# Kernel optimization log

Hardware: AMD Instinct MI355X
Metric: run time of the kernel (lower is better)

## Reference

```python
import jax, jax.numpy as jnp
import numpy as np

B, N, T, S = 32, 102400, 64, 1600
PI = float(np.pi)
EPS = 1e-12  # numerical guard inside sqrt for cdist (diagonal is exactly 0)


def _cdist(a, b):
    # a: (..., P, 3), b: (..., Q, 3) -> (..., P, Q) euclidean distances
    sq = jnp.sum((a[..., :, None, :] - b[..., None, :, :]) ** 2, axis=-1)
    return jnp.sqrt(sq + EPS)


def _rigid_t(alpha, trans, sz, center):
    # alpha, trans: (B, T, 3). Returns XYZ (B,T,3,3), translation (B,T,3).
    c, s = jnp.cos(alpha), jnp.sin(alpha)
    z = jnp.zeros_like(c[..., 0]); o = jnp.ones_like(c[..., 0])
    X = jnp.stack([c[..., 0], -s[..., 0], z, s[..., 0], c[..., 0], z, z, z, o], -1).reshape(*alpha.shape[:2], 3, 3)
    Y = jnp.stack([c[..., 1], z, s[..., 1], z, o, z, -s[..., 1], z, c[..., 1]], -1).reshape(*alpha.shape[:2], 3, 3)
    Z = jnp.stack([o, z, z, z, c[..., 2], -s[..., 2], z, s[..., 2], c[..., 2]], -1).reshape(*alpha.shape[:2], 3, 3)
    XYZ = jnp.einsum('btij,btjk,btkl->btil', X, Y, Z)
    eye = jnp.eye(3, dtype=alpha.dtype)
    Tt = trans * sz[None, None, :] + jnp.einsum('m,btmk->btk', center, eye[None, None] - XYZ)
    return XYZ, Tt


def setup_inputs():
    key = jax.random.key(0)
    ks = jax.random.split(key, 6)
    x = jax.random.normal(ks[0], (B, 6, N), jnp.float32)
    w1 = jax.random.normal(ks[1], (3 * N, 32), jnp.float32) * 0.005
    b1 = jnp.zeros((32,), jnp.float32)
    w2 = jax.random.normal(ks[2], (32, 6 * T), jnp.float32) * 0.05
    b2 = jnp.zeros((6 * T,), jnp.float32)
    A = jax.random.normal(ks[3], (6, N), jnp.float32)
    mask = jax.random.uniform(ks[4], (T, T), jnp.float32)
    sz = jnp.array([128.0, 128.0, 64.0], jnp.float32)
    tess = jnp.arange(N, dtype=jnp.int32).reshape(T, S)  # equal-size partition
    return {'x': x, 'w1': w1, 'b1': b1, 'w2': w2, 'b2': b2, 'A': A, 'mask': mask, 'sz': sz, 'tess': tess}


def reference(x, w1, b1, w2, b2, A, mask, sz, tess):
    center = sz / 2.0
    # localization MLP on flattened xyz coords: (B, 3N) -> (B, T, 6)
    xflat = x[:, :3, :].reshape(B, 3 * N)
    h = jax.nn.relu(xflat @ w1 + b1)
    z_l = jnp.tanh(h @ w2 + b2).reshape(B, T, 6)
    # NOTE: original code uses z_l[:, :, 3:] for BOTH angles and translation
    r_, t_ = _rigid_t(PI * z_l[:, :, 3:], z_l[:, :, 3:], sz, center)
    x3 = x[:, :3, :]
    xg = x3[:, :, tess]  # gather: (B, 3, T, S)
    # out[b,j,p,n] = sum_k r_[b,p,k,j] * xg[b,k,p,n]  (matches einsum 'bkt,bkn->btn')
    rot = jnp.einsum('bpkj,bkpn->bjpn', r_, xg) + t_.transpose(0, 2, 1)[:, :, :, None]
    # scatter back into full point cloud (tess partitions N)
    X3 = jnp.zeros_like(x3).at[:, :, tess.reshape(-1)].set(rot.reshape(B, 3, N))
    X_t = jnp.concatenate([X3, x[:, 3:, :]], axis=1)  # colors pass through identity
    # regularizer on per-piece centroids
    pts_1 = A[:3][:, tess].mean(axis=2).T                 # (T, 3)
    pts_2 = X3[:, :, tess].mean(axis=3).transpose(0, 2, 1)  # (B, T, 3)
    diff = _cdist(pts_1, pts_1)[None] - _cdist(pts_2, pts_2)
    reg = jnp.sum((mask[None] * diff) ** 2, axis=(1, 2))  # (B,)
    return X_t, reg
```

## Files before the change

### kernel.cpp

```cpp
#include <hip/hip_runtime.h>
#include <hip/hip_bf16.h>
#include <math.h>

#define BB 32
#define NN 102400
#define TT 64
#define SS 1600
#define K3N (3 * NN)
#define KC 128
#define G1 512
#define NCHUNK (K3N / KC)
#define XPAD 132
#define PI_F 3.14159265358979323846f

__global__ __launch_bounds__(256) void k1_gemm(const float* __restrict__ x,
                                               const float* __restrict__ w1,
                                               float* __restrict__ h_part) {
    __shared__ float xs[32 * XPAD];
    __shared__ float ws1[KC * 32];
    const int tid = threadIdx.x;
    const int b = tid >> 3, cq = tid & 7;
    float a0 = 0.f, a1 = 0.f, a2 = 0.f, a3 = 0.f;

    for (int chunk = blockIdx.x; chunk < NCHUNK; chunk += G1) {
        const int k0 = chunk * KC;
        for (int i = tid; i < 32 * 32; i += 256) {
            const int bb = i >> 5, k4 = i & 31;
            const float4 v = *(const float4*)(x + (size_t)bb * 6 * NN + k0 + k4 * 4);
            *(float4*)(xs + bb * XPAD + k4 * 4) = v;
        }
        for (int i = tid; i < (KC * 32) / 4; i += 256) {
            *(float4*)(ws1 + i * 4) = *(const float4*)(w1 + (size_t)k0 * 32 + i * 4);
        }
        __syncthreads();
        const float* xrow = xs + b * XPAD;
        #pragma unroll 8
        for (int k4 = 0; k4 < KC / 4; ++k4) {
            const float4 xv = *(const float4*)(xrow + k4 * 4);
            #pragma unroll
            for (int j = 0; j < 4; ++j) {
                const float xj = j == 0 ? xv.x : (j == 1 ? xv.y : (j == 2 ? xv.z : xv.w));
                const float4 wv = *(const float4*)(ws1 + (k4 * 4 + j) * 32 + cq * 4);
                a0 = fmaf(xj, wv.x, a0);
                a1 = fmaf(xj, wv.y, a1);
                a2 = fmaf(xj, wv.z, a2);
                a3 = fmaf(xj, wv.w, a3);
            }
        }
        __syncthreads();
    }
    float4 r; r.x = a0; r.y = a1; r.z = a2; r.w = a3;
    *(float4*)(h_part + (size_t)blockIdx.x * 1024 + tid * 4) = r;
}

__global__ __launch_bounds__(256) void kb_fused(const float* __restrict__ h_part,
                                                const float* __restrict__ b1,
                                                const float* __restrict__ w2,
                                                const float* __restrict__ b2,
                                                const float* __restrict__ sz,
                                                const float* __restrict__ A,
                                                const int* __restrict__ tess,
                                                float* __restrict__ RT,
                                                float* __restrict__ pts1) {
    const int blk = blockIdx.x;
    if (blk < BB) {
        const int bb = blk;
        __shared__ float part[8][32];
        __shared__ float hsh[32];
        const int c = threadIdx.x & 31, g = threadIdx.x >> 5;
        float s = 0.f;
        for (int j = g; j < G1; j += 8) s += h_part[(size_t)j * 1024 + bb * 32 + c];
        part[g][c] = s;
        __syncthreads();
        if (threadIdx.x < 32) {
            float acc = 0.f;
            #pragma unroll
            for (int g2 = 0; g2 < 8; ++g2) acc += part[g2][threadIdx.x];
            hsh[threadIdx.x] = fmaxf(acc + b1[threadIdx.x], 0.f);
        }
        __syncthreads();
        const int t = threadIdx.x;
        if (t < TT) {
            float z[3];
            #pragma unroll
            for (int j = 0; j < 3; ++j) {
                const int col = 6 * t + 3 + j;
                float s2 = b2[col];
                #pragma unroll 8
                for (int cc = 0; cc < 32; ++cc) s2 = fmaf(hsh[cc], w2[cc * 384 + col], s2);
                z[j] = tanhf(s2);
            }
            float c0, s0, c1, s1, c2, s2v;
            sincosf(PI_F * z[0], &s0, &c0);
            sincosf(PI_F * z[1], &s1, &c1);
            sincosf(PI_F * z[2], &s2v, &c2);
            const float R00 = c0 * c1;
            const float R01 = -s0 * c2 + c0 * s1 * s2v;
            const float R02 = s0 * s2v + c0 * s1 * c2;
            const float R10 = s0 * c1;
            const float R11 = c0 * c2 + s0 * s1 * s2v;
            const float R12 = -c0 * s2v + s0 * s1 * c2;
            const float R20 = -s1;
            const float R21 = c1 * s2v;
            const float R22 = c1 * c2;
            const float szx = sz[0], szy = sz[1], szz = sz[2];
            const float cx = 0.5f * szx, cy = 0.5f * szy, cz = 0.5f * szz;
            const float T0 = z[0] * szx + cx - (cx * R00 + cy * R10 + cz * R20);
            const float T1 = z[1] * szy + cy - (cx * R01 + cy * R11 + cz * R21);
            const float T2 = z[2] * szz + cz - (cx * R02 + cy * R12 + cz * R22);
            float* o = RT + (bb * TT + t) * 12;
            o[0] = R00; o[1] = R10; o[2]  = R20; o[3]  = T0;
            o[4] = R01; o[5] = R11; o[6]  = R21; o[7]  = T1;
            o[8] = R02; o[9] = R12; o[10] = R22; o[11] = T2;
        }
    } else {
        const int t = blk - BB;
        const int* tr = tess + t * SS;
        float s0 = 0.f, s1 = 0.f, s2 = 0.f;
        for (int s = threadIdx.x; s < SS; s += 256) {
            const int idx = tr[s];
            s0 += A[idx]; s1 += A[NN + idx]; s2 += A[2 * NN + idx];
        }
        #pragma unroll
        for (int o = 32; o > 0; o >>= 1) {
            s0 += __shfl_down(s0, o, 64);
            s1 += __shfl_down(s1, o, 64);
            s2 += __shfl_down(s2, o, 64);
        }
        __shared__ float red[4 * 3];
        const int lane = threadIdx.x & 63, wv = threadIdx.x >> 6;
        if (lane == 0) { red[wv * 3] = s0; red[wv * 3 + 1] = s1; red[wv * 3 + 2] = s2; }
        __syncthreads();
        if (threadIdx.x < 3) {
            const float s = red[threadIdx.x] + red[3 + threadIdx.x] + red[6 + threadIdx.x] + red[9 + threadIdx.x];
            pts1[t * 3 + threadIdx.x] = s * (1.0f / SS);
        }
    }
}

__global__ __launch_bounds__(256) void k3_transform(const float* __restrict__ x,
                                                    const int* __restrict__ tess,
                                                    const float* __restrict__ RT,
                                                    float* __restrict__ out,
                                                    float* __restrict__ pts2) {
    const int blk = blockIdx.x;
    const int b = blk / TT, t = blk % TT;
    const float* p = RT + blk * 12;
    const float M00 = p[0], M01 = p[1], M02 = p[2], T0 = p[3];
    const float M10 = p[4], M11 = p[5], M12 = p[6], T1 = p[7];
    const float M20 = p[8], M21 = p[9], M22 = p[10], T2 = p[11];
    const float* xb = x + (size_t)b * 6 * NN;
    float* ob = out + (size_t)b * 6 * NN;
    const int* tr = tess + t * SS;
    float s0 = 0.f, s1 = 0.f, s2 = 0.f;
    for (int s = threadIdx.x; s < SS; s += 256) {
        const int idx = tr[s];
        const float x0 = xb[idx], x1 = xb[NN + idx], x2 = xb[2 * NN + idx];
        const float y0 = fmaf(M00, x0, fmaf(M01, x1, fmaf(M02, x2, T0)));
        const float y1 = fmaf(M10, x0, fmaf(M11, x1, fmaf(M12, x2, T1)));
        const float y2 = fmaf(M20, x0, fmaf(M21, x1, fmaf(M22, x2, T2)));
        ob[idx] = y0; ob[NN + idx] = y1; ob[2 * NN + idx] = y2;
        s0 += y0; s1 += y1; s2 += y2;
    }
    const int n0 = t * SS;
    for (int i = threadIdx.x; i < 1200; i += 256) {
        const int ch = i / 400, r = i - ch * 400;
        const size_t off = (size_t)(3 + ch) * NN + n0 + r * 4;
        *(float4*)(ob + off) = *(const float4*)(xb + off);
    }
    #pragma unroll
    for (int o = 32; o > 0; o >>= 1) {
        s0 += __shfl_down(s0, o, 64);
        s1 += __shfl_down(s1, o, 64);
        s2 += __shfl_down(s2, o, 64);
    }
    __shared__ float red[4 * 3];
    const int lane = threadIdx.x & 63, wv = threadIdx.x >> 6;
    if (lane == 0) { red[wv * 3] = s0; red[wv * 3 + 1] = s1; red[wv * 3 + 2] = s2; }
    __syncthreads();
    if (threadIdx.x < 3) {
        const float s = red[threadIdx.x] + red[3 + threadIdx.x] + red[6 + threadIdx.x] + red[9 + threadIdx.x];
        pts2[blk * 3 + threadIdx.x] = s * (1.0f / SS);
    }
}

__global__ __launch_bounds__(256) void k5_reg(const float* __restrict__ pts1,
                                              const float* __restrict__ pts2,
                                              const float* __restrict__ mask,
                                              float* __restrict__ out) {
    const int b = blockIdx.x;
    __shared__ float p1[TT * 3], p2[TT * 3];
    for (int i = threadIdx.x; i < TT * 3; i += 256) {
        p1[i] = pts1[i];
        p2[i] = pts2[b * TT * 3 + i];
    }
    __syncthreads();
    float acc = 0.f;
    for (int pr = threadIdx.x; pr < TT * TT; pr += 256) {
        const int t = pr >> 6, u = pr & 63;
        float dx = p1[t * 3] - p1[u * 3];
        float dy = p1[t * 3 + 1] - p1[u * 3 + 1];
        float dz = p1[t * 3 + 2] - p1[u * 3 + 2];
        const float d1 = sqrtf(dx * dx + dy * dy + dz * dz + 1e-12f);
        dx = p2[t * 3] - p2[u * 3];
        dy = p2[t * 3 + 1] - p2[u * 3 + 1];
        dz = p2[t * 3 + 2] - p2[u * 3 + 2];
        const float d2 = sqrtf(dx * dx + dy * dy + dz * dz + 1e-12f);
        const float d = mask[pr] * (d1 - d2);
        acc = fmaf(d, d, acc);
    }
    #pragma unroll
    for (int o = 32; o > 0; o >>= 1) acc += __shfl_down(acc, o, 64);
    __shared__ float red[4];
    const int lane = threadIdx.x & 63, wv = threadIdx.x >> 6;
    if (lane == 0) red[wv] = acc;
    __syncthreads();
    if (threadIdx.x == 0) {
        out[(size_t)BB * 6 * NN + b] = red[0] + red[1] + red[2] + red[3];
    }
}

extern "C" void kernel_launch(void* const* d_in, const int* in_sizes, int n_in,
                              void* d_out, int out_size, void* d_ws, size_t ws_size,
                              hipStream_t stream) {
    const float* x    = (const float*)d_in[0];
    const float* w1   = (const float*)d_in[1];
    const float* b1   = (const float*)d_in[2];
    const float* w2   = (const float*)d_in[3];
    const float* b2   = (const float*)d_in[4];
    const float* A    = (const float*)d_in[5];
    const float* mask = (const float*)d_in[6];
    const float* sz   = (const float*)d_in[7];
    const int*   tess = (const int*)d_in[8];
    float* out = (float*)d_out;
    float* ws  = (float*)d_ws;

    float* h_part = ws;
    float* RT     = h_part + G1 * 1024;
    float* pts2   = RT + BB * TT * 12;
    float* pts1   = pts2 + BB * TT * 3;

    k1_gemm<<<G1, 256, 0, stream>>>(x, w1, h_part);
    kb_fused<<<BB + TT, 256, 0, stream>>>(h_part, b1, w2, b2, sz, A, tess, RT, pts1);
    k3_transform<<<BB * TT, 256, 0, stream>>>(x, tess, RT, out, pts2);
    k5_reg<<<BB, 256, 0, stream>>>(pts1, pts2, mask, out);
}
```

Measured before the change: 90.07 us.

## Retile first GEMM with 4x8 register tiles, split-K across lanes, larger grid

```diff
diff --git a/kernel.cpp b/kernel.cpp
--- a/kernel.cpp
+++ b/kernel.cpp
@@ -7,50 +7,84 @@
 #define TT 64
 #define SS 1600
 #define K3N (3 * NN)
-#define KC 128
-#define G1 512
+#define KC 64
 #define NCHUNK (K3N / KC)
-#define XPAD 132
+#define XP 68
+#define WP 40
 #define PI_F 3.14159265358979323846f
 
 __global__ __launch_bounds__(256) void k1_gemm(const float* __restrict__ x,
                                                const float* __restrict__ w1,
                                                float* __restrict__ h_part) {
-    __shared__ float xs[32 * XPAD];
-    __shared__ float ws1[KC * 32];
+    __shared__ float xs[32 * XP];
+    __shared__ float ws1[KC * WP];
     const int tid = threadIdx.x;
-    const int b = tid >> 3, cq = tid & 7;
-    float a0 = 0.f, a1 = 0.f, a2 = 0.f, a3 = 0.f;
-
-    for (int chunk = blockIdx.x; chunk < NCHUNK; chunk += G1) {
+    const int ks = tid & 7;
+    const int tile = tid >> 3;
+    const int bg = tile & 7;
+    const int cg = tile >> 3;
+    float acc[4][8];
+    #pragma unroll
+    for (int j = 0; j < 4; ++j)
+        #pragma unroll
+        for (int c = 0; c < 8; ++c) acc[j][c] = 0.f;
+
+    const int nblk = gridDim.x;
+    for (int chunk = blockIdx.x; chunk < NCHUNK; chunk += nblk) {
         const int k0 = chunk * KC;
-        for (int i = tid; i < 32 * 32; i += 256) {
-            const int bb = i >> 5, k4 = i & 31;
-            const float4 v = *(const float4*)(x + (size_t)bb * 6 * NN + k0 + k4 * 4);
-            *(float4*)(xs + bb * XPAD + k4 * 4) = v;
-        }
-        for (int i = tid; i < (KC * 32) / 4; i += 256) {
-            *(float4*)(ws1 + i * 4) = *(const float4*)(w1 + (size_t)k0 * 32 + i * 4);
-        }
-        __syncthreads();
-        const float* xrow = xs + b * XPAD;
-        #pragma unroll 8
-        for (int k4 = 0; k4 < KC / 4; ++k4) {
-            const float4 xv = *(const float4*)(xrow + k4 * 4);
+        {
+            const int bb = tid >> 4, k4 = (tid & 15) * 4;
+            const float4 v0 = *(const float4*)(x + (size_t)bb * 6 * NN + k0 + k4);
+            *(float4*)(xs + bb * XP + k4) = v0;
+            const float4 v1 = *(const float4*)(x + (size_t)(bb + 16) * 6 * NN + k0 + k4);
+            *(float4*)(xs + (bb + 16) * XP + k4) = v1;
+        }
+        {
+            const int r = tid >> 3, c4 = (tid & 7) * 4;
+            *(float4*)(ws1 + r * WP + c4) = *(const float4*)(w1 + (size_t)(k0 + r) * 32 + c4);
+            *(float4*)(ws1 + (r + 32) * WP + c4) = *(const float4*)(w1 + (size_t)(k0 + r + 32) * 32 + c4);
+        }
+        __syncthreads();
+        #pragma unroll
+        for (int i = 0; i < 8; ++i) {
+            const int k = ks + 8 * i;
+            const float4 wa = *(const float4*)(ws1 + k * WP + cg * 8);
+            const float4 wb = *(const float4*)(ws1 + k * WP + cg * 8 + 4);
+            float xv[4];
+            #pragma unroll
+            for (int j = 0; j < 4; ++j) xv[j] = xs[(bg + 8 * j) * XP + k];
             #pragma unroll
             for (int j = 0; j < 4; ++j) {
-                const float xj = j == 0 ? xv.x : (j == 1 ? xv.y : (j == 2 ? xv.z : xv.w));
-                const float4 wv = *(const float4*)(ws1 + (k4 * 4 + j) * 32 + cq * 4);
-                a0 = fmaf(xj, wv.x, a0);
-                a1 = fmaf(xj, wv.y, a1);
-                a2 = fmaf(xj, wv.z, a2);
-                a3 = fmaf(xj, wv.w, a3);
+                acc[j][0] = fmaf(xv[j], wa.x, acc[j][0]);
+                acc[j][1] = fmaf(xv[j], wa.y, acc[j][1]);
+                acc[j][2] = fmaf(xv[j], wa.z, acc[j][2]);
+                acc[j][3] = fmaf(xv[j], wa.w, acc[j][3]);
+                acc[j][4] = fmaf(xv[j], wb.x, acc[j][4]);
+                acc[j][5] = fmaf(xv[j], wb.y, acc[j][5]);
+                acc[j][6] = fmaf(xv[j], wb.z, acc[j][6]);
+                acc[j][7] = fmaf(xv[j], wb.w, acc[j][7]);
             }
         }
         __syncthreads();
     }
-    float4 r; r.x = a0; r.y = a1; r.z = a2; r.w = a3;
-    *(float4*)(h_part + (size_t)blockIdx.x * 1024 + tid * 4) = r;
+    #pragma unroll
+    for (int off = 1; off < 8; off <<= 1) {
+        #pragma unroll
+        for (int j = 0; j < 4; ++j)
+            #pragma unroll
+            for (int c = 0; c < 8; ++c)
+                acc[j][c] += __shfl_xor(acc[j][c], off, 64);
+    }
+    if (ks == 0) {
+        float* hp = h_part + (size_t)blockIdx.x * 1024;
+        #pragma unroll
+        for (int j = 0; j < 4; ++j) {
+            const int b = bg + 8 * j;
+            #pragma unroll
+            for (int c = 0; c < 8; ++c)
+                hp[b * 32 + cg * 8 + c] = acc[j][c];
+        }
+    }
 }
 
 __global__ __launch_bounds__(256) void kb_fused(const float* __restrict__ h_part,
@@ -61,7 +95,8 @@
                                                 const float* __restrict__ A,
                                                 const int* __restrict__ tess,
                                                 float* __restrict__ RT,
-                                                float* __restrict__ pts1) {
+                                                float* __restrict__ pts1,
+                                                int g1) {
     const int blk = blockIdx.x;
     if (blk < BB) {
         const int bb = blk;
@@ -69,7 +104,7 @@
         __shared__ float hsh[32];
         const int c = threadIdx.x & 31, g = threadIdx.x >> 5;
         float s = 0.f;
-        for (int j = g; j < G1; j += 8) s += h_part[(size_t)j * 1024 + bb * 32 + c];
+        for (int j = g; j < g1; j += 8) s += h_part[(size_t)j * 1024 + bb * 32 + c];
         part[g][c] = s;
         __syncthreads();
         if (threadIdx.x < 32) {
@@ -235,13 +270,16 @@
     float* out = (float*)d_out;
     float* ws  = (float*)d_ws;
 
+    int g1 = 1024;
+    while ((size_t)(g1 * 1024 + 2048 * 12 + 2048 * 3 + 192) * 4 > ws_size && g1 > 128) g1 >>= 1;
+
     float* h_part = ws;
-    float* RT     = h_part + G1 * 1024;
+    float* RT     = h_part + (size_t)g1 * 1024;
     float* pts2   = RT + BB * TT * 12;
     float* pts1   = pts2 + BB * TT * 3;
 
-    k1_gemm<<<G1, 256, 0, stream>>>(x, w1, h_part);
-    kb_fused<<<BB + TT, 256, 0, stream>>>(h_part, b1, w2, b2, sz, A, tess, RT, pts1);
+    k1_gemm<<<g1, 256, 0, stream>>>(x, w1, h_part);
+    kb_fused<<<BB + TT, 256, 0, stream>>>(h_part, b1, w2, b2, sz, A, tess, RT, pts1, g1);
     k3_transform<<<BB * TT, 256, 0, stream>>>(x, tess, RT, out, pts2);
     k5_reg<<<BB, 256, 0, stream>>>(pts1, pts2, mask, out);
 }
```

Result: slower. 95.83 us (+6.4%).

## Restructure GEMM as per-wave split-K and fuse color copy and centroids into it

Applied to the files above, without the earlier changes.

```diff
diff --git a/kernel.cpp b/kernel.cpp
--- a/kernel.cpp
+++ b/kernel.cpp
@@ -7,134 +7,149 @@
 #define TT 64
 #define SS 1600
 #define K3N (3 * NN)
-#define KC 128
-#define G1 512
-#define NCHUNK (K3N / KC)
-#define XPAD 132
+#define CPB 512
 #define PI_F 3.14159265358979323846f
 
-__global__ __launch_bounds__(256) void k1_gemm(const float* __restrict__ x,
+__global__ __launch_bounds__(256) void k1_mega(const float* __restrict__ x,
                                                const float* __restrict__ w1,
-                                               float* __restrict__ h_part) {
-    __shared__ float xs[32 * XPAD];
-    __shared__ float ws1[KC * 32];
+                                               const float* __restrict__ A,
+                                               const int* __restrict__ tess,
+                                               float* __restrict__ h_part,
+                                               float* __restrict__ out,
+                                               float* __restrict__ pts1,
+                                               int nw) {
     const int tid = threadIdx.x;
-    const int b = tid >> 3, cq = tid & 7;
-    float a0 = 0.f, a1 = 0.f, a2 = 0.f, a3 = 0.f;
-
-    for (int chunk = blockIdx.x; chunk < NCHUNK; chunk += G1) {
-        const int k0 = chunk * KC;
-        for (int i = tid; i < 32 * 32; i += 256) {
-            const int bb = i >> 5, k4 = i & 31;
-            const float4 v = *(const float4*)(x + (size_t)bb * 6 * NN + k0 + k4 * 4);
-            *(float4*)(xs + bb * XPAD + k4 * 4) = v;
-        }
-        for (int i = tid; i < (KC * 32) / 4; i += 256) {
-            *(float4*)(ws1 + i * 4) = *(const float4*)(w1 + (size_t)k0 * 32 + i * 4);
-        }
+    const int gemmBlocks = nw >> 2;
+    if (blockIdx.x < gemmBlocks) {
+        const int wid = blockIdx.x * 4 + (tid >> 6);
+        const int lane = tid & 63;
+        const int b = lane & 31, kh = lane >> 5;
+        const int kstart = (int)(((long)wid * K3N) / nw);
+        const int kend   = (int)(((long)(wid + 1) * K3N) / nw);
+
+        float acc[32];
+        #pragma unroll
+        for (int c = 0; c < 32; ++c) acc[c] = 0.f;
+
+        const float* xp = x + (size_t)b * 6 * NN + kstart + kh;
+        const float* wp = w1 + (size_t)(kstart + kh) * 32;
+
+        #pragma unroll 2
+        for (int k0 = kstart; k0 < kend; k0 += 2) {
+            const float xv = *xp;
+            float4 w[8];
+            #pragma unroll
+            for (int q = 0; q < 8; ++q) w[q] = *(const float4*)(wp + 4 * q);
+            #pragma unroll
+            for (int q = 0; q < 8; ++q) {
+                acc[4 * q + 0] = fmaf(xv, w[q].x, acc[4 * q + 0]);
+                acc[4 * q + 1] = fmaf(xv, w[q].y, acc[4 * q + 1]);
+                acc[4 * q + 2] = fmaf(xv, w[q].z, acc[4 * q + 2]);
+                acc[4 * q + 3] = fmaf(xv, w[q].w, acc[4 * q + 3]);
+            }
+            xp += 2;
+            wp += 64;
+        }
+        #pragma unroll
+        for (int c = 0; c < 32; ++c) acc[c] += __shfl_xor(acc[c], 32, 64);
+        if (kh == 0) {
+            float* hp = h_part + (size_t)wid * 1024 + b * 32;
+            #pragma unroll
+            for (int q = 0; q < 8; ++q) {
+                float4 v;
+                v.x = acc[4 * q + 0]; v.y = acc[4 * q + 1];
+                v.z = acc[4 * q + 2]; v.w = acc[4 * q + 3];
+                *(float4*)(hp + 4 * q) = v;
+            }
+        }
+    } else if (blockIdx.x < gemmBlocks + CPB) {
+        const int cb = blockIdx.x - gemmBlocks;
+        for (int i = cb * 256 + tid; i < 2457600; i += CPB * 256) {
+            const int b = i / 76800;
+            const int rem = i - b * 76800;
+            const size_t off = (size_t)b * (6 * NN) + K3N + (size_t)rem * 4;
+            *(float4*)(out + off) = *(const float4*)(x + off);
+        }
+    } else {
+        const int t = blockIdx.x - gemmBlocks - CPB;
+        const int* tr = tess + t * SS;
+        float s0 = 0.f, s1 = 0.f, s2 = 0.f;
+        for (int s = tid; s < SS; s += 256) {
+            const int idx = tr[s];
+            s0 += A[idx]; s1 += A[NN + idx]; s2 += A[2 * NN + idx];
+        }
+        #pragma unroll
+        for (int o = 32; o > 0; o >>= 1) {
+            s0 += __shfl_down(s0, o, 64);
+            s1 += __shfl_down(s1, o, 64);
+            s2 += __shfl_down(s2, o, 64);
+        }
+        __shared__ float red[4 * 3];
+        const int lane = tid & 63, wv = tid >> 6;
+        if (lane == 0) { red[wv * 3] = s0; red[wv * 3 + 1] = s1; red[wv * 3 + 2] = s2; }
         __syncthreads();
-        const float* xrow = xs + b * XPAD;
-        #pragma unroll 8
-        for (int k4 = 0; k4 < KC / 4; ++k4) {
-            const float4 xv = *(const float4*)(xrow + k4 * 4);
-            #pragma unroll
-            for (int j = 0; j < 4; ++j) {
-                const float xj = j == 0 ? xv.x : (j == 1 ? xv.y : (j == 2 ? xv.z : xv.w));
-                const float4 wv = *(const float4*)(ws1 + (k4 * 4 + j) * 32 + cq * 4);
-                a0 = fmaf(xj, wv.x, a0);
-                a1 = fmaf(xj, wv.y, a1);
-                a2 = fmaf(xj, wv.z, a2);
-                a3 = fmaf(xj, wv.w, a3);
-            }
-        }
-        __syncthreads();
-    }
-    float4 r; r.x = a0; r.y = a1; r.z = a2; r.w = a3;
-    *(float4*)(h_part + (size_t)blockIdx.x * 1024 + tid * 4) = r;
-}
-
-__global__ __launch_bounds__(256) void kb_fused(const float* __restrict__ h_part,
+        if (tid < 3) {
+            const float s = red[tid] + red[3 + tid] + red[6 + tid] + red[9 + tid];
+            pts1[t * 3 + tid] = s * (1.0f / SS);
+        }
+    }
+}
+
+__global__ __launch_bounds__(256) void kb_rigid(const float* __restrict__ h_part,
                                                 const float* __restrict__ b1,
                                                 const float* __restrict__ w2,
                                                 const float* __restrict__ b2,
                                                 const float* __restrict__ sz,
-                                                const float* __restrict__ A,
-                                                const int* __restrict__ tess,
                                                 float* __restrict__ RT,
-                                                float* __restrict__ pts1) {
-    const int blk = blockIdx.x;
-    if (blk < BB) {
-        const int bb = blk;
-        __shared__ float part[8][32];
-        __shared__ float hsh[32];
-        const int c = threadIdx.x & 31, g = threadIdx.x >> 5;
-        float s = 0.f;
-        for (int j = g; j < G1; j += 8) s += h_part[(size_t)j * 1024 + bb * 32 + c];
-        part[g][c] = s;
-        __syncthreads();
-        if (threadIdx.x < 32) {
-            float acc = 0.f;
-            #pragma unroll
-            for (int g2 = 0; g2 < 8; ++g2) acc += part[g2][threadIdx.x];
-            hsh[threadIdx.x] = fmaxf(acc + b1[threadIdx.x], 0.f);
-        }
-        __syncthreads();
-        const int t = threadIdx.x;
-        if (t < TT) {
-            float z[3];
-            #pragma unroll
-            for (int j = 0; j < 3; ++j) {
-                const int col = 6 * t + 3 + j;
-                float s2 = b2[col];
-                #pragma unroll 8
-                for (int cc = 0; cc < 32; ++cc) s2 = fmaf(hsh[cc], w2[cc * 384 + col], s2);
-                z[j] = tanhf(s2);
-            }
-            float c0, s0, c1, s1, c2, s2v;
-            sincosf(PI_F * z[0], &s0, &c0);
-            sincosf(PI_F * z[1], &s1, &c1);
-            sincosf(PI_F * z[2], &s2v, &c2);
-            const float R00 = c0 * c1;
-            const float R01 = -s0 * c2 + c0 * s1 * s2v;
-            const float R02 = s0 * s2v + c0 * s1 * c2;
-            const float R10 = s0 * c1;
-            const float R11 = c0 * c2 + s0 * s1 * s2v;
-            const float R12 = -c0 * s2v + s0 * s1 * c2;
-            const float R20 = -s1;
-            const float R21 = c1 * s2v;
-            const float R22 = c1 * c2;
-            const float szx = sz[0], szy = sz[1], szz = sz[2];
-            const float cx = 0.5f * szx, cy = 0.5f * szy, cz = 0.5f * szz;
-            const float T0 = z[0] * szx + cx - (cx * R00 + cy * R10 + cz * R20);
-            const float T1 = z[1] * szy + cy - (cx * R01 + cy * R11 + cz * R21);
-            const float T2 = z[2] * szz + cz - (cx * R02 + cy * R12 + cz * R22);
-            float* o = RT + (bb * TT + t) * 12;
-            o[0] = R00; o[1] = R10; o[2]  = R20; o[3]  = T0;
-            o[4] = R01; o[5] = R11; o[6]  = R21; o[7]  = T1;
-            o[8] = R02; o[9] = R12; o[10] = R22; o[11] = T2;
-        }
-    } else {
-        const int t = blk - BB;
-        const int* tr = tess + t * SS;
-        float s0 = 0.f, s1 = 0.f, s2 = 0.f;
-        for (int s = threadIdx.x; s < SS; s += 256) {
-            const int idx = tr[s];
-            s0 += A[idx]; s1 += A[NN + idx]; s2 += A[2 * NN + idx];
-        }
-        #pragma unroll
-        for (int o = 32; o > 0; o >>= 1) {
-            s0 += __shfl_down(s0, o, 64);
-            s1 += __shfl_down(s1, o, 64);
-            s2 += __shfl_down(s2, o, 64);
-        }
-        __shared__ float red[4 * 3];
-        const int lane = threadIdx.x & 63, wv = threadIdx.x >> 6;
-        if (lane == 0) { red[wv * 3] = s0; red[wv * 3 + 1] = s1; red[wv * 3 + 2] = s2; }
-        __syncthreads();
-        if (threadIdx.x < 3) {
-            const float s = red[threadIdx.x] + red[3 + threadIdx.x] + red[6 + threadIdx.x] + red[9 + threadIdx.x];
-            pts1[t * 3 + threadIdx.x] = s * (1.0f / SS);
-        }
+                                                int nw) {
+    const int bb = blockIdx.x;
+    __shared__ float part[8][32];
+    __shared__ float hsh[32];
+    const int c = threadIdx.x & 31, g = threadIdx.x >> 5;
+    float s = 0.f;
+    for (int j = g; j < nw; j += 8) s += h_part[(size_t)j * 1024 + bb * 32 + c];
+    part[g][c] = s;
+    __syncthreads();
+    if (threadIdx.x < 32) {
+        float acc = 0.f;
+        #pragma unroll
+        for (int g2 = 0; g2 < 8; ++g2) acc += part[g2][threadIdx.x];
+        hsh[threadIdx.x] = fmaxf(acc + b1[threadIdx.x], 0.f);
+    }
+    __syncthreads();
+    const int t = threadIdx.x;
+    if (t < TT) {
+        float z[3];
+        #pragma unroll
+        for (int j = 0; j < 3; ++j) {
+            const int col = 6 * t + 3 + j;
+            float s2 = b2[col];
+            #pragma unroll 8
+            for (int cc = 0; cc < 32; ++cc) s2 = fmaf(hsh[cc], w2[cc * 384 + col], s2);
+            z[j] = tanhf(s2);
+        }
+        float c0, s0, c1, s1, c2, s2v;
+        sincosf(PI_F * z[0], &s0, &c0);
+        sincosf(PI_F * z[1], &s1, &c1);
+        sincosf(PI_F * z[2], &s2v, &c2);
+        const float R00 = c0 * c1;
+        const float R01 = -s0 * c2 + c0 * s1 * s2v;
+        const float R02 = s0 * s2v + c0 * s1 * c2;
+        const float R10 = s0 * c1;
+        const float R11 = c0 * c2 + s0 * s1 * s2v;
+        const float R12 = -c0 * s2v + s0 * s1 * c2;
+        const float R20 = -s1;
+        const float R21 = c1 * s2v;
+        const float R22 = c1 * c2;
+        const float szx = sz[0], szy = sz[1], szz = sz[2];
+        const float cx = 0.5f * szx, cy = 0.5f * szy, cz = 0.5f * szz;
+        const float T0 = z[0] * szx + cx - (cx * R00 + cy * R10 + cz * R20);
+        const float T1 = z[1] * szy + cy - (cx * R01 + cy * R11 + cz * R21);
+        const float T2 = z[2] * szz + cz - (cx * R02 + cy * R12 + cz * R22);
+        float* o = RT + (bb * TT + t) * 12;
+        o[0] = R00; o[1] = R10; o[2]  = R20; o[3]  = T0;
+        o[4] = R01; o[5] = R11; o[6]  = R21; o[7]  = T1;
+        o[8] = R02; o[9] = R12; o[10] = R22; o[11] = T2;
     }
 }
 
@@ -162,12 +177,6 @@
         ob[idx] = y0; ob[NN + idx] = y1; ob[2 * NN + idx] = y2;
         s0 += y0; s1 += y1; s2 += y2;
     }
-    const int n0 = t * SS;
-    for (int i = threadIdx.x; i < 1200; i += 256) {
-        const int ch = i / 400, r = i - ch * 400;
-        const size_t off = (size_t)(3 + ch) * NN + n0 + r * 4;
-        *(float4*)(ob + off) = *(const float4*)(xb + off);
-    }
     #pragma unroll
     for (int o = 32; o > 0; o >>= 1) {
         s0 += __shfl_down(s0, o, 64);
@@ -235,13 +244,16 @@
     float* out = (float*)d_out;
     float* ws  = (float*)d_ws;
 
+    int nw = 2048;
+    while ((size_t)((size_t)nw * 1024 + 2048 * 12 + 2048 * 3 + 192) * 4 > ws_size && nw > 512) nw >>= 1;
+
     float* h_part = ws;
-    float* RT     = h_part + G1 * 1024;
+    float* RT     = h_part + (size_t)nw * 1024;
     float* pts2   = RT + BB * TT * 12;
     float* pts1   = pts2 + BB * TT * 3;
 
-    k1_gemm<<<G1, 256, 0, stream>>>(x, w1, h_part);
-    kb_fused<<<BB + TT, 256, 0, stream>>>(h_part, b1, w2, b2, sz, A, tess, RT, pts1);
+    k1_mega<<<(nw >> 2) + CPB + TT, 256, 0, stream>>>(x, w1, A, tess, h_part, out, pts1, nw);
+    kb_rigid<<<BB, 256, 0, stream>>>(h_part, b1, w2, b2, sz, RT, nw);
     k3_transform<<<BB * TT, 256, 0, stream>>>(x, tess, RT, out, pts2);
     k5_reg<<<BB, 256, 0, stream>>>(pts1, pts2, mask, out);
 }
```

Result: slower. 166.6 us (+84.9%).
